# Performance work log

Hardware: AMD Instinct MI355X
Metric: run time of the kernel (lower is better)

The kernel has to match this reference:

```python
import jax, jax.numpy as jnp
import numpy as np

HQ, HKV, D = 16, 2, 128   # num_heads_q, num_heads_kv, head_dim
G = HQ // HKV             # q heads per kv head (repeat_interleave factor)


def setup_inputs() -> dict:
    key = jax.random.key(0)
    ks = jax.random.split(key, 6)
    B, T, C = 2, 2048, 2048
    def w(k, shape):
        return jax.random.normal(k, shape, jnp.float32) * (1.0 / np.sqrt(shape[0]).astype(np.float32))
    x = jax.random.normal(ks[0], (B, T, C), jnp.float32)
    Wq = w(ks[1], (C, HQ * D))
    Wk = w(ks[2], (C, HKV * D))
    Wv = w(ks[3], (C, HKV * D))
    Wo = w(ks[4], (HQ * D, C))
    Wg = w(ks[5], (C, HQ))
    # causal mask: True where attention is disallowed (j > i)
    mask = jnp.triu(jnp.ones((T, T), dtype=bool), k=1)[None, None]  # (1,1,T,T)
    return {"x": x, "mask": mask, "Wq": Wq, "Wk": Wk, "Wv": Wv, "Wo": Wo, "Wg": Wg}


def reference(x, mask, Wq, Wk, Wv, Wo, Wg):
    B, T, C = x.shape
    # repeat_interleave(G, dim=heads) means q head h uses kv head h // G,
    # so group q heads as (HKV, G) instead of materializing repeated K/V.
    q = (x @ Wq).reshape(B, T, HKV, G, D).transpose(0, 2, 3, 1, 4)  # (B,HKV,G,T,D)
    k = (x @ Wk).reshape(B, T, HKV, D).transpose(0, 2, 1, 3)        # (B,HKV,T,D)
    v = (x @ Wv).reshape(B, T, HKV, D).transpose(0, 2, 1, 3)        # (B,HKV,T,D)
    scale = jnp.float32(1.0 / np.sqrt(D))
    scores = jnp.einsum('bkgtd,bksd->bkgts', q, k) * scale          # (B,HKV,G,T,T)
    scores = jnp.where(mask[:, None], jnp.float32(-1e9), scores)    # causal fill
    attn = jax.nn.softmax(scores, axis=-1)
    # post-softmax sigmoid gate, one scalar per (batch, q-head, query token)
    gates = jax.nn.sigmoid(x @ Wg)                                   # (B,T,HQ)
    gates = gates.transpose(0, 2, 1).reshape(B, HKV, G, T)           # (B,HKV,G,T)
    out = jnp.einsum('bkgts,bksd->btkgd', attn * gates[..., None], v)
    out = out.reshape(B, T, HQ * D)
    return out @ Wo
```

## Files before the change

kernel.cpp:

```cpp
#include <hip/hip_runtime.h>
#include <hip/hip_bf16.h>
#include <math.h>

#define HQ 16
#define HKV 2
#define D 128
#define B_SZ 2
#define T_SZ 2048
#define C_SZ 2048
#define QKVN 2688

#define C_Q 0.12753102f
#define C_G 1.44269504f

typedef __attribute__((ext_vector_type(8))) short short8;
typedef __attribute__((ext_vector_type(4))) float floatx4;

static __device__ __forceinline__ float fexp2(float x) {
    return __builtin_amdgcn_exp2f(x);
}

static __device__ __forceinline__ unsigned short f2b(float f) {
    union { float f; unsigned u; } x; x.f = f;
    return (unsigned short)((x.u + 0x7fffu + ((x.u >> 16) & 1u)) >> 16);
}

static __device__ __forceinline__ unsigned int pk2(float a, float b) {
    float2 t; t.x = a; t.y = b;
    __hip_bfloat162 h = __float22bfloat162_rn(t);
    return *(unsigned int*)&h;
}

static __device__ __forceinline__ void load_lds16(const void* g, void* l) {
    __builtin_amdgcn_global_load_lds(
        (const __attribute__((address_space(1))) void*)g,
        (__attribute__((address_space(3))) void*)l,
        16, 0, 0);
}

static __device__ __forceinline__ void tr32(
    const float* __restrict__ in, unsigned short* __restrict__ out,
    int R, int Cc, float premul, int bx, int by, float (*t)[33])
{
    const int bc = bx * 32, br = by * 32;
    const int tid = threadIdx.x;
    const int r = tid >> 3, c4 = (tid & 7) * 4;
    float4 v = *(const float4*)(in + (size_t)(br + r) * Cc + bc + c4);
    t[r][c4 + 0] = v.x; t[r][c4 + 1] = v.y; t[r][c4 + 2] = v.z; t[r][c4 + 3] = v.w;
    __syncthreads();
    ushort4 o;
    o.x = f2b(t[c4 + 0][r] * premul); o.y = f2b(t[c4 + 1][r] * premul);
    o.z = f2b(t[c4 + 2][r] * premul); o.w = f2b(t[c4 + 3][r] * premul);
    *(ushort4*)(out + (size_t)(bc + r) * R + br + c4) = o;
}

__global__ __launch_bounds__(256) void prep_kernel(
    const float* __restrict__ x,  const float* __restrict__ Wq,
    const float* __restrict__ Wk, const float* __restrict__ Wv,
    const float* __restrict__ Wo, const float* __restrict__ Wg,
    unsigned short* __restrict__ xb, unsigned short* __restrict__ Wqkvt,
    unsigned short* __restrict__ Wot)
{
    __shared__ float t[32][33];
    const int bid = blockIdx.x;
    const int tid = threadIdx.x;
    if (bid < 4096) {
        int i = bid * 2048 + tid * 8;
        float4 a = *(const float4*)(x + i);
        float4 b = *(const float4*)(x + i + 4);
        ushort4 o0, o1;
        o0.x = f2b(a.x); o0.y = f2b(a.y); o0.z = f2b(a.z); o0.w = f2b(a.w);
        o1.x = f2b(b.x); o1.y = f2b(b.y); o1.z = f2b(b.z); o1.w = f2b(b.w);
        *(ushort4*)(xb + i) = o0;
        *(ushort4*)(xb + i + 4) = o1;
    } else if (bid < 8192) {
        int n = bid - 4096;
        tr32(Wq, Wqkvt, C_SZ, HQ * D, C_Q, n & 63, n >> 6, t);
    } else if (bid < 8704) {
        int n = bid - 8192;
        tr32(Wk, Wqkvt + (size_t)(HQ * D) * C_SZ, C_SZ, HKV * D, 1.0f, n & 7, n >> 3, t);
    } else if (bid < 9216) {
        int n = bid - 8704;
        tr32(Wv, Wqkvt + (size_t)(HQ * D + HKV * D) * C_SZ, C_SZ, HKV * D, 1.0f, n & 7, n >> 3, t);
    } else if (bid < 13312) {
        int n = bid - 9216;
        tr32(Wo, Wot, HQ * D, C_SZ, 1.0f, n & 63, n >> 6, t);
    } else {
        int k = (bid - 13312) * 256 + tid;
        const float4* wr = (const float4*)(Wg + (size_t)k * 16);
        float4 w0 = wr[0], w1 = wr[1], w2 = wr[2], w3 = wr[3];
        float w[16] = {w0.x, w0.y, w0.z, w0.w, w1.x, w1.y, w1.z, w1.w,
                       w2.x, w2.y, w2.z, w2.w, w3.x, w3.y, w3.z, w3.w};
        unsigned short* out = Wqkvt + (size_t)(HQ * D + 2 * HKV * D) * C_SZ;
        #pragma unroll
        for (int h = 0; h < 16; ++h)
            out[(size_t)h * C_SZ + k] = f2b(w[h] * C_G);
    }
}

template<int BM>
__global__ __launch_bounds__(512, 2) void gemm256(
    const unsigned short* __restrict__ A, const unsigned short* __restrict__ Bt,
    float* __restrict__ Cf, unsigned short* __restrict__ Cb,
    unsigned short* __restrict__ Vt, int Nreal, int K, int out_bf16)
{
    constexpr int MT = BM / 32;
    constexpr int LA = BM / 64;
    constexpr int VM = LA + 4;
    __shared__ __align__(16) unsigned short SM[2][(BM + 256) * 64];

    const int tid = threadIdx.x;
    const int lane = tid & 63, wave = tid >> 6;
    const int l15 = lane & 15, quad = lane >> 4;
    const int wm = wave >> 2, wn = wave & 3;
    const int bm0 = blockIdx.y * BM, bn0 = blockIdx.x * 256;
    const int NT = K >> 6;

    unsigned aoff[LA], boff[4];
    #pragma unroll
    for (int j = 0; j < LA; ++j) {
        int c = j * 512 + tid, r = c >> 3, sb = c & 7;
        aoff[j] = (unsigned)(((bm0 + r) * K + ((sb ^ (r & 7)) << 3)) * 2);
    }
    #pragma unroll
    for (int j = 0; j < 4; ++j) {
        int c = j * 512 + tid, r = c >> 3, sb = c & 7;
        boff[j] = (unsigned)(((bn0 + r) * K + ((sb ^ (r & 7)) << 3)) * 2);
    }

    floatx4 zero = {0.f, 0.f, 0.f, 0.f};
    floatx4 acc[MT][4];
    #pragma unroll
    for (int i = 0; i < MT; ++i)
        #pragma unroll
        for (int j = 0; j < 4; ++j) acc[i][j] = zero;

    auto STAGE = [&](int b, int t) {
        #pragma unroll
        for (int j = 0; j < LA; ++j)
            load_lds16((const char*)A + aoff[j] + (size_t)t * 128,
                       &SM[b][(j * 512 + wave * 64) * 8]);
        #pragma unroll
        for (int j = 0; j < 4; ++j)
            load_lds16((const char*)Bt + boff[j] + (size_t)t * 128,
                       &SM[b][BM * 64 + (j * 512 + wave * 64) * 8]);
    };

    auto RD = [&](short8 (&FA)[MT], short8 (&FB)[4], int b, int kk) {
        const unsigned short* Sa = &SM[b][0];
        const unsigned short* Sb = &SM[b][BM * 64];
        const int swz = ((kk << 2) + quad) ^ (l15 & 7);
        #pragma unroll
        for (int mt = 0; mt < MT; ++mt)
            FA[mt] = *(const short8*)&Sa[(wm * (BM / 2) + mt * 16 + l15) * 64 + swz * 8];
        #pragma unroll
        for (int nt = 0; nt < 4; ++nt)
            FB[nt] = *(const short8*)&Sb[(wn * 64 + nt * 16 + l15) * 64 + swz * 8];
    };

    auto MM = [&](short8 (&FA)[MT], short8 (&FB)[4]) {
        __builtin_amdgcn_s_setprio(1);
        #pragma unroll
        for (int mt = 0; mt < MT; ++mt)
            #pragma unroll
            for (int nt = 0; nt < 4; ++nt)
                acc[mt][nt] = __builtin_amdgcn_mfma_f32_16x16x32_bf16(
                    FA[mt], FB[nt], acc[mt][nt], 0, 0, 0);
        __builtin_amdgcn_s_setprio(0);
    };

    short8 RaA[MT], RaB[4], RbA[MT], RbB[4];

    STAGE(0, 0);
    STAGE(1, 1);
    asm volatile("s_waitcnt vmcnt(%0)" :: "n"(VM) : "memory");
    __builtin_amdgcn_sched_barrier(0);
    __builtin_amdgcn_s_barrier();
    __builtin_amdgcn_sched_barrier(0);
    RD(RaA, RaB, 0, 0);

    #pragma unroll 2
    for (int t = 0; t < NT; ++t) {
        const int b = t & 1;
        RD(RbA, RbB, b, 1);
        MM(RaA, RaB);
        asm volatile("s_waitcnt lgkmcnt(0)" ::: "memory");
        __builtin_amdgcn_sched_barrier(0);
        __builtin_amdgcn_s_barrier();
        __builtin_amdgcn_sched_barrier(0);
        if (t + 2 < NT) {
            STAGE(b, t + 2);
            asm volatile("s_waitcnt vmcnt(%0)" :: "n"(VM) : "memory");
        } else if (t + 1 < NT) {
            asm volatile("s_waitcnt vmcnt(0)" ::: "memory");
        }
        __builtin_amdgcn_sched_barrier(0);
        __builtin_amdgcn_s_barrier();
        __builtin_amdgcn_sched_barrier(0);
        if (t + 1 < NT) RD(RaA, RaB, b ^ 1, 0);
        MM(RbA, RbB);
    }

    if (Vt != nullptr && bn0 == 2304) {
        unsigned short (*Ct)[264] = (unsigned short(*)[264])SM;
        const int bb = bm0 >> 11;
        const int tl = bm0 & 2047;
        #pragma unroll
        for (int v = 0; v < 4; ++v) {
            __syncthreads();
            if (wn == v) {
                #pragma unroll
                for (int mt = 0; mt < MT; ++mt)
                    #pragma unroll
                    for (int nt = 0; nt < 4; ++nt)
                        #pragma unroll
                        for (int r = 0; r < 4; ++r)
                            Ct[nt * 16 + l15][wm * (BM / 2) + mt * 16 + quad * 4 + r] =
                                f2b(acc[mt][nt][r]);
            }
            __syncthreads();
            int row = tid >> 3, c0 = (tid & 7) * 32;
            unsigned short* dst = Vt + ((size_t)bb * (HKV * D) + v * 64 + row) * T_SZ
                                     + tl + c0;
            const unsigned short* src = &Ct[row][c0];
            short8 s0 = *(const short8*)(src + 0);
            short8 s1 = *(const short8*)(src + 8);
            short8 s2 = *(const short8*)(src + 16);
            short8 s3 = *(const short8*)(src + 24);
            *(short8*)(dst + 0)  = s0; *(short8*)(dst + 8)  = s1;
            *(short8*)(dst + 16) = s2; *(short8*)(dst + 24) = s3;
        }
        return;
    }

    #pragma unroll
    for (int mt = 0; mt < MT; ++mt)
        #pragma unroll
        for (int nt = 0; nt < 4; ++nt) {
            const int n = bn0 + wn * 64 + nt * 16 + l15;
            if (n < Nreal) {
                #pragma unroll
                for (int r = 0; r < 4; ++r) {
                    const int m = bm0 + wm * (BM / 2) + mt * 16 + quad * 4 + r;
                    if (out_bf16) Cb[(size_t)m * Nreal + n] = f2b(acc[mt][nt][r]);
                    else          Cf[(size_t)m * Nreal + n] = acc[mt][nt][r];
                }
            }
        }
}

__global__ __launch_bounds__(256, 3) void attn_mfma(
    const unsigned short* __restrict__ QKV, const unsigned short* __restrict__ Vt,
    unsigned short* __restrict__ Ob)
{
    __shared__ __align__(16) unsigned short SMEM[64 * 128 + 128 * 64 + 4 * 16 * 72];
    unsigned short* Ks = SMEM;
    unsigned short* Vs = SMEM + 64 * 128;
    unsigned short* Ps = SMEM + 64 * 128 + 128 * 64;
    unsigned short* Lo = SMEM;

    const int bh = blockIdx.x;
    const int qt = (int)gridDim.y - 1 - (int)blockIdx.y;
    const int b = bh >> 4, h = bh & 15, kvh = h >> 3;
    const int tid = threadIdx.x;
    const int lane = tid & 63, w = tid >> 6;
    const int l15 = lane & 15, quad = lane >> 4;
    const int q_local = w * 16 + l15;
    const float BIAS = 32.0f;

    short8 aq[4];
    {
        const unsigned short* qp = QKV + (size_t)(b * T_SZ + qt * 64 + q_local) * QKVN
                                       + h * D + quad * 8;
        #pragma unroll
        for (int kd = 0; kd < 4; ++kd) aq[kd] = *(const short8*)(qp + kd * 32);
    }

    const unsigned short* kg[4];
    const unsigned short* vg[4];
    #pragma unroll
    for (int it = 0; it < 4; ++it) {
        int Bi = it * 256 + tid;
        int kr = Bi >> 4, kc = ((Bi & 15) ^ (kr & 15)) * 8;
        kg[it] = QKV + (size_t)(b * T_SZ + kr) * QKVN + HQ * D + kvh * D + kc;
        int vr = Bi >> 3, vc = ((Bi & 7) ^ (vr & 7)) * 8;
        vg[it] = Vt + (size_t)((b * HKV + kvh) * D + vr) * T_SZ + vc;
    }

    floatx4 zero = {0.f, 0.f, 0.f, 0.f};
    floatx4 oacc[8];
    #pragma unroll
    for (int dt = 0; dt < 8; ++dt) oacc[dt] = zero;
    float l_part = 0.f;

    short8 krg[4], vrg[4];
    #pragma unroll
    for (int it = 0; it < 4; ++it) {
        krg[it] = *(const short8*)(kg[it]);
        vrg[it] = *(const short8*)(vg[it]);
    }

    for (int kt = 0; kt <= qt; ++kt) {
        asm volatile("s_waitcnt vmcnt(0)" ::: "memory");
        __builtin_amdgcn_sched_barrier(0);
        __builtin_amdgcn_s_barrier();
        __builtin_amdgcn_sched_barrier(0);
        #pragma unroll
        for (int it = 0; it < 4; ++it) {
            *(short8*)&Ks[(it * 256 + tid) * 8] = krg[it];
            *(short8*)&Vs[(it * 256 + tid) * 8] = vrg[it];
        }
        if (kt < qt) {
            #pragma unroll
            for (int it = 0; it < 4; ++it) {
                krg[it] = *(const short8*)(kg[it] + (size_t)(kt + 1) * 64 * QKVN);
                vrg[it] = *(const short8*)(vg[it] + (kt + 1) * 64);
            }
        }
        asm volatile("s_waitcnt lgkmcnt(0)" ::: "memory");
        __builtin_amdgcn_sched_barrier(0);
        __builtin_amdgcn_s_barrier();
        __builtin_amdgcn_sched_barrier(0);

        floatx4 sacc[4];
        #pragma unroll
        for (int nt = 0; nt < 4; ++nt) sacc[nt] = zero;
        #pragma unroll
        for (int kd = 0; kd < 4; ++kd)
            #pragma unroll
            for (int nt = 0; nt < 4; ++nt) {
                short8 ak = *(const short8*)&Ks[((nt * 16 + l15) * 16 + ((kd * 4 + quad) ^ l15)) * 8];
                sacc[nt] = __builtin_amdgcn_mfma_f32_16x16x32_bf16(ak, aq[kd], sacc[nt], 0, 0, 0);
            }

        float p[4][4];
        if (kt == qt) {
            #pragma unroll
            for (int nt = 0; nt < 4; ++nt)
                #pragma unroll
                for (int r = 0; r < 4; ++r) {
                    float e = fexp2(sacc[nt][r] - BIAS);
                    p[nt][r] = (nt * 16 + quad * 4 + r > q_local) ? 0.f : e;
                }
        } else {
            #pragma unroll
            for (int nt = 0; nt < 4; ++nt)
                #pragma unroll
                for (int r = 0; r < 4; ++r)
                    p[nt][r] = fexp2(sacc[nt][r] - BIAS);
        }
        #pragma unroll
        for (int nt = 0; nt < 4; ++nt) {
            l_part += (p[nt][0] + p[nt][1]) + (p[nt][2] + p[nt][3]);
            uint2 pw;
            pw.x = pk2(p[nt][0], p[nt][1]);
            pw.y = pk2(p[nt][2], p[nt][3]);
            *(uint2*)&Ps[(w * 16 + l15) * 72 + nt * 16 + quad * 4] = pw;
        }

        #pragma unroll
        for (int kk = 0; kk < 2; ++kk) {
            short8 bp = *(const short8*)&Ps[(w * 16 + l15) * 72 + kk * 32 + quad * 8];
            #pragma unroll
            for (int dt = 0; dt < 8; ++dt) {
                short8 av = *(const short8*)&Vs[((dt * 16 + l15) * 8 + ((kk * 4 + quad) ^ (l15 & 7))) * 8];
                oacc[dt] = __builtin_amdgcn_mfma_f32_16x16x32_bf16(av, bp, oacc[dt], 0, 0, 0);
            }
        }
    }

    float l = l_part;
    l += __shfl_xor(l, 16);
    l += __shfl_xor(l, 32);

    __syncthreads();
    {
        int token = b * T_SZ + qt * 64 + q_local;
        unsigned short gl = QKV[(size_t)token * QKVN + HQ * D + HKV * D * 2 + h];
        union { unsigned u; float f; } gx; gx.u = ((unsigned)gl) << 16;
        float g = 1.0f / (1.0f + fexp2(-gx.f));
        float f = g / l;
        #pragma unroll
        for (int dt = 0; dt < 8; ++dt) {
            uint2 ov;
            ov.x = pk2(oacc[dt][0] * f, oacc[dt][1] * f);
            ov.y = pk2(oacc[dt][2] * f, oacc[dt][3] * f);
            *(uint2*)&Lo[(size_t)q_local * 136 + dt * 16 + quad * 4] = ov;
        }
    }
    __syncthreads();
    {
        int row = tid >> 2, c0 = (tid & 3) * 32;
        size_t tok = (size_t)(b * T_SZ + qt * 64 + row);
        unsigned short* op = Ob + tok * (HQ * D) + h * D + c0;
        const unsigned short* lp = &Lo[(size_t)row * 136 + c0];
        short8 v0 = *(const short8*)(lp + 0);
        short8 v1 = *(const short8*)(lp + 8);
        short8 v2 = *(const short8*)(lp + 16);
        short8 v3 = *(const short8*)(lp + 24);
        *(short8*)(op + 0)  = v0; *(short8*)(op + 8)  = v1;
        *(short8*)(op + 16) = v2; *(short8*)(op + 24) = v3;
    }
}

extern "C" void kernel_launch(void* const* d_in, const int* in_sizes, int n_in,
                              void* d_out, int out_size, void* d_ws, size_t ws_size,
                              hipStream_t stream) {
    const float* x  = (const float*)d_in[0];
    const float* Wq = (const float*)d_in[2];
    const float* Wk = (const float*)d_in[3];
    const float* Wv = (const float*)d_in[4];
    const float* Wo = (const float*)d_in[5];
    const float* Wg = (const float*)d_in[6];
    float* out = (float*)d_out;

    const size_t KB = 1ull << 10;
    char* p = (char*)d_ws;
    unsigned short* xb    = (unsigned short*)(p);
    unsigned short* Ob    = xb;
    unsigned short* Wqkvt = (unsigned short*)(p + 16384 * KB);
    unsigned short* Wot   = (unsigned short*)(p + 27136 * KB);
    unsigned short* QKV   = (unsigned short*)(p + 35328 * KB);
    unsigned short* Vt    = (unsigned short*)(p + 56832 * KB);
    const int BT = B_SZ * T_SZ;

    prep_kernel<<<dim3(13320), 256, 0, stream>>>(x, Wq, Wk, Wv, Wo, Wg, xb, Wqkvt, Wot);

    gemm256<256><<<dim3(11, BT / 256), 512, 0, stream>>>(
        xb, Wqkvt, nullptr, QKV, Vt, QKVN, C_SZ, 1);

    attn_mfma<<<dim3(B_SZ * HQ, T_SZ / 64), 256, 0, stream>>>(QKV, Vt, Ob);

    gemm256<128><<<dim3(C_SZ / 256, BT / 128), 512, 0, stream>>>(
        Ob, Wot, out, nullptr, nullptr, C_SZ, HQ * D, 0);
}
```

Measured before the change: 289.8 us.

## Restructure GEMM into quadrant ping-pong pipeline and load attention K/V directly to LDS

The GEMM kernel is rebuilt so each K step is split into four quadrant MFMA phases. Loads for the next A and B halves are interleaved between those phases, and workgroup IDs are remapped so neighbouring tiles land on the same XCD. The attention kernel drops its register prefetch of K/V and instead issues direct global-to-LDS loads each iteration, with its occupancy hint relaxed. This aims to overlap global traffic with MFMA work and improve L2 locality in the GEMMs. In exchange it adds many more barriers per step, and the attention loop no longer overlaps the next tile's fetch with compute.

```diff
diff --git a/kernel.cpp b/kernel.cpp
--- a/kernel.cpp
+++ b/kernel.cpp
@@ -37,6 +37,8 @@
         (__attribute__((address_space(3))) void*)l,
         16, 0, 0);
 }
+
+#define SBAR __builtin_amdgcn_sched_barrier(0)
 
 static __device__ __forceinline__ void tr32(
     const float* __restrict__ in, unsigned short* __restrict__ out,
@@ -99,34 +101,54 @@
 }
 
 template<int BM>
-__global__ __launch_bounds__(512, 2) void gemm256(
+__global__ __launch_bounds__(512, 2) void gemm8p(
     const unsigned short* __restrict__ A, const unsigned short* __restrict__ Bt,
     float* __restrict__ Cf, unsigned short* __restrict__ Cb,
     unsigned short* __restrict__ Vt, int Nreal, int K, int out_bf16)
 {
     constexpr int MT = BM / 32;
-    constexpr int LA = BM / 64;
+    constexpr int MH = MT / 2;
+    constexpr int LA = BM / 128;
+    constexpr int AUNIT = (BM / 2) * 64;
+    constexpr int BUNIT = 8192;
+    constexpr int BUF = 2 * AUNIT + 2 * BUNIT;
     constexpr int VM = LA + 4;
-    __shared__ __align__(16) unsigned short SM[2][(BM + 256) * 64];
+    __shared__ __align__(16) unsigned short SM[2][BUF];
 
     const int tid = threadIdx.x;
     const int lane = tid & 63, wave = tid >> 6;
     const int l15 = lane & 15, quad = lane >> 4;
     const int wm = wave >> 2, wn = wave & 3;
-    const int bm0 = blockIdx.y * BM, bn0 = blockIdx.x * 256;
     const int NT = K >> 6;
 
-    unsigned aoff[LA], boff[4];
-    #pragma unroll
-    for (int j = 0; j < LA; ++j) {
-        int c = j * 512 + tid, r = c >> 3, sb = c & 7;
-        aoff[j] = (unsigned)(((bm0 + r) * K + ((sb ^ (r & 7)) << 3)) * 2);
-    }
-    #pragma unroll
-    for (int j = 0; j < 4; ++j) {
-        int c = j * 512 + tid, r = c >> 3, sb = c & 7;
-        boff[j] = (unsigned)(((bn0 + r) * K + ((sb ^ (r & 7)) << 3)) * 2);
-    }
+    const int nwg = (int)(gridDim.x * gridDim.y);
+    int flat = (int)(blockIdx.y * gridDim.x + blockIdx.x);
+    const int cpx = nwg >> 3;
+    flat = (flat & 7) * cpx + (flat >> 3);
+    const int bm0 = (flat / (int)gridDim.x) * BM;
+    const int bn0 = (flat % (int)gridDim.x) * 256;
+
+    const int rr = tid >> 3;
+    const int cb8 = ((tid & 7) ^ (rr & 7)) << 3;
+    unsigned aoff[2][LA], boff[2][2];
+    #pragma unroll
+    for (int mh = 0; mh < 2; ++mh)
+        #pragma unroll
+        for (int j = 0; j < LA; ++j) {
+            int row_l = j * 64 + rr;
+            int grow;
+            if (BM == 256) grow = bm0 + (row_l >> 6) * 128 + mh * 64 + (row_l & 63);
+            else           grow = bm0 + (row_l >> 5) * 64  + mh * 32 + (row_l & 31);
+            aoff[mh][j] = (unsigned)((grow * K + cb8) * 2);
+        }
+    #pragma unroll
+    for (int nh = 0; nh < 2; ++nh)
+        #pragma unroll
+        for (int j = 0; j < 2; ++j) {
+            int row_l = j * 64 + rr;
+            int gnr = bn0 + (row_l >> 5) * 64 + nh * 32 + (row_l & 31);
+            boff[nh][j] = (unsigned)((gnr * K + cb8) * 2);
+        }
 
     floatx4 zero = {0.f, 0.f, 0.f, 0.f};
     floatx4 acc[MT][4];
@@ -135,73 +157,93 @@
         #pragma unroll
         for (int j = 0; j < 4; ++j) acc[i][j] = zero;
 
-    auto STAGE = [&](int b, int t) {
+    auto STAGE_A = [&](int b, int mh, int t) {
         #pragma unroll
         for (int j = 0; j < LA; ++j)
-            load_lds16((const char*)A + aoff[j] + (size_t)t * 128,
-                       &SM[b][(j * 512 + wave * 64) * 8]);
-        #pragma unroll
-        for (int j = 0; j < 4; ++j)
-            load_lds16((const char*)Bt + boff[j] + (size_t)t * 128,
-                       &SM[b][BM * 64 + (j * 512 + wave * 64) * 8]);
+            load_lds16((const char*)A + aoff[mh][j] + (size_t)t * 128,
+                       &SM[b][mh * AUNIT + (j * 512 + wave * 64) * 8]);
     };
-
-    auto RD = [&](short8 (&FA)[MT], short8 (&FB)[4], int b, int kk) {
-        const unsigned short* Sa = &SM[b][0];
-        const unsigned short* Sb = &SM[b][BM * 64];
-        const int swz = ((kk << 2) + quad) ^ (l15 & 7);
-        #pragma unroll
-        for (int mt = 0; mt < MT; ++mt)
-            FA[mt] = *(const short8*)&Sa[(wm * (BM / 2) + mt * 16 + l15) * 64 + swz * 8];
-        #pragma unroll
-        for (int nt = 0; nt < 4; ++nt)
-            FB[nt] = *(const short8*)&Sb[(wn * 64 + nt * 16 + l15) * 64 + swz * 8];
+    auto STAGE_B = [&](int b, int nh, int t) {
+        #pragma unroll
+        for (int j = 0; j < 2; ++j)
+            load_lds16((const char*)Bt + boff[nh][j] + (size_t)t * 128,
+                       &SM[b][2 * AUNIT + nh * BUNIT + (j * 512 + wave * 64) * 8]);
     };
 
-    auto MM = [&](short8 (&FA)[MT], short8 (&FB)[4]) {
+    short8 fa[MH][2], fb[4][2];
+    auto RD_A = [&](int b, int mh) {
+        const unsigned short* Sa = &SM[b][mh * AUNIT];
+        #pragma unroll
+        for (int i = 0; i < MH; ++i) {
+            const int row_l = wm * (BM / 4) + i * 16 + l15;
+            #pragma unroll
+            for (int kk = 0; kk < 2; ++kk)
+                fa[i][kk] = *(const short8*)&Sa[row_l * 64 +
+                    ((((kk << 2) + quad) ^ (l15 & 7)) << 3)];
+        }
+    };
+    auto RD_Bh = [&](int b, int nh) {
+        const unsigned short* Sb = &SM[b][2 * AUNIT + nh * BUNIT];
+        #pragma unroll
+        for (int s = 0; s < 2; ++s) {
+            const int row_l = wn * 32 + s * 16 + l15;
+            #pragma unroll
+            for (int kk = 0; kk < 2; ++kk)
+                fb[nh * 2 + s][kk] = *(const short8*)&Sb[row_l * 64 +
+                    ((((kk << 2) + quad) ^ (l15 & 7)) << 3)];
+        }
+    };
+    auto MMQ = [&](int mh, int nh) {
         __builtin_amdgcn_s_setprio(1);
         #pragma unroll
-        for (int mt = 0; mt < MT; ++mt)
-            #pragma unroll
-            for (int nt = 0; nt < 4; ++nt)
-                acc[mt][nt] = __builtin_amdgcn_mfma_f32_16x16x32_bf16(
-                    FA[mt], FB[nt], acc[mt][nt], 0, 0, 0);
+        for (int i = 0; i < MH; ++i)
+            #pragma unroll
+            for (int s = 0; s < 2; ++s)
+                #pragma unroll
+                for (int kk = 0; kk < 2; ++kk)
+                    acc[mh * MH + i][nh * 2 + s] = __builtin_amdgcn_mfma_f32_16x16x32_bf16(
+                        fa[i][kk], fb[nh * 2 + s][kk], acc[mh * MH + i][nh * 2 + s], 0, 0, 0);
         __builtin_amdgcn_s_setprio(0);
     };
 
-    short8 RaA[MT], RaB[4], RbA[MT], RbB[4];
-
-    STAGE(0, 0);
-    STAGE(1, 1);
+    STAGE_A(0, 0, 0); STAGE_B(0, 0, 0); STAGE_B(0, 1, 0); STAGE_A(0, 1, 0);
+    if (NT > 1) { STAGE_A(1, 0, 1); STAGE_B(1, 0, 1); STAGE_B(1, 1, 1); }
     asm volatile("s_waitcnt vmcnt(%0)" :: "n"(VM) : "memory");
-    __builtin_amdgcn_sched_barrier(0);
-    __builtin_amdgcn_s_barrier();
-    __builtin_amdgcn_sched_barrier(0);
-    RD(RaA, RaB, 0, 0);
+    SBAR; __builtin_amdgcn_s_barrier(); SBAR;
 
     #pragma unroll 2
     for (int t = 0; t < NT; ++t) {
         const int b = t & 1;
-        RD(RbA, RbB, b, 1);
-        MM(RaA, RaB);
-        asm volatile("s_waitcnt lgkmcnt(0)" ::: "memory");
-        __builtin_amdgcn_sched_barrier(0);
-        __builtin_amdgcn_s_barrier();
-        __builtin_amdgcn_sched_barrier(0);
+        RD_A(b, 0); RD_Bh(b, 0);
+        if (t + 1 < NT) STAGE_A(b ^ 1, 1, t + 1);
+        SBAR; __builtin_amdgcn_s_barrier(); SBAR;
+        asm volatile("s_waitcnt lgkmcnt(0)" ::: "memory"); SBAR;
+        MMQ(0, 0);
+        SBAR; __builtin_amdgcn_s_barrier(); SBAR;
+        RD_Bh(b, 1);
+        if (t + 2 < NT) STAGE_A(b, 0, t + 2);
+        SBAR; __builtin_amdgcn_s_barrier(); SBAR;
+        asm volatile("s_waitcnt lgkmcnt(0)" ::: "memory"); SBAR;
+        MMQ(0, 1);
+        SBAR; __builtin_amdgcn_s_barrier(); SBAR;
+        RD_A(b, 1);
+        if (t + 2 < NT) STAGE_B(b, 0, t + 2);
+        SBAR; __builtin_amdgcn_s_barrier(); SBAR;
+        asm volatile("s_waitcnt lgkmcnt(0)" ::: "memory"); SBAR;
+        MMQ(1, 1);
+        SBAR; __builtin_amdgcn_s_barrier(); SBAR;
         if (t + 2 < NT) {
-            STAGE(b, t + 2);
+            STAGE_B(b, 1, t + 2);
             asm volatile("s_waitcnt vmcnt(%0)" :: "n"(VM) : "memory");
-        } else if (t + 1 < NT) {
+        } else {
             asm volatile("s_waitcnt vmcnt(0)" ::: "memory");
         }
-        __builtin_amdgcn_sched_barrier(0);
-        __builtin_amdgcn_s_barrier();
-        __builtin_amdgcn_sched_barrier(0);
-        if (t + 1 < NT) RD(RaA, RaB, b ^ 1, 0);
-        MM(RbA, RbB);
-    }
-
-    if (Vt != nullptr && bn0 == 2304) {
+        SBAR; __builtin_amdgcn_s_barrier(); SBAR;
+        MMQ(1, 0);
+        SBAR; __builtin_amdgcn_s_barrier(); SBAR;
+    }
+
+    if (BM == 256 && Vt != nullptr && bn0 == 2304) {
         unsigned short (*Ct)[264] = (unsigned short(*)[264])SM;
         const int bb = bm0 >> 11;
         const int tl = bm0 & 2047;
@@ -249,7 +291,7 @@
         }
 }
 
-__global__ __launch_bounds__(256, 3) void attn_mfma(
+__global__ __launch_bounds__(256) void attn_mfma(
     const unsigned short* __restrict__ QKV, const unsigned short* __restrict__ Vt,
     unsigned short* __restrict__ Ob)
 {
@@ -293,34 +335,14 @@
     for (int dt = 0; dt < 8; ++dt) oacc[dt] = zero;
     float l_part = 0.f;
 
-    short8 krg[4], vrg[4];
-    #pragma unroll
-    for (int it = 0; it < 4; ++it) {
-        krg[it] = *(const short8*)(kg[it]);
-        vrg[it] = *(const short8*)(vg[it]);
-    }
-
     for (int kt = 0; kt <= qt; ++kt) {
-        asm volatile("s_waitcnt vmcnt(0)" ::: "memory");
-        __builtin_amdgcn_sched_barrier(0);
-        __builtin_amdgcn_s_barrier();
-        __builtin_amdgcn_sched_barrier(0);
+        __syncthreads();
         #pragma unroll
         for (int it = 0; it < 4; ++it) {
-            *(short8*)&Ks[(it * 256 + tid) * 8] = krg[it];
-            *(short8*)&Vs[(it * 256 + tid) * 8] = vrg[it];
-        }
-        if (kt < qt) {
-            #pragma unroll
-            for (int it = 0; it < 4; ++it) {
-                krg[it] = *(const short8*)(kg[it] + (size_t)(kt + 1) * 64 * QKVN);
-                vrg[it] = *(const short8*)(vg[it] + (kt + 1) * 64);
-            }
-        }
-        asm volatile("s_waitcnt lgkmcnt(0)" ::: "memory");
-        __builtin_amdgcn_sched_barrier(0);
-        __builtin_amdgcn_s_barrier();
-        __builtin_amdgcn_sched_barrier(0);
+            load_lds16(kg[it] + (size_t)kt * 64 * QKVN, &Ks[(it * 256 + w * 64) * 8]);
+            load_lds16(vg[it] + kt * 64,                &Vs[(it * 256 + w * 64) * 8]);
+        }
+        __syncthreads();
 
         floatx4 sacc[4];
         #pragma unroll
@@ -426,11 +448,11 @@
 
     prep_kernel<<<dim3(13320), 256, 0, stream>>>(x, Wq, Wk, Wv, Wo, Wg, xb, Wqkvt, Wot);
 
-    gemm256<256><<<dim3(11, BT / 256), 512, 0, stream>>>(
+    gemm8p<256><<<dim3(11, BT / 256), 512, 0, stream>>>(
         xb, Wqkvt, nullptr, QKV, Vt, QKVN, C_SZ, 1);
 
     attn_mfma<<<dim3(B_SZ * HQ, T_SZ / 64), 256, 0, stream>>>(QKV, Vt, Ob);
 
-    gemm256<128><<<dim3(C_SZ / 256, BT / 128), 512, 0, stream>>>(
+    gemm8p<128><<<dim3(8, BT / 128), 512, 0, stream>>>(
         Ob, Wot, out, nullptr, nullptr, C_SZ, HQ * D, 0);
 }
```

Result: faster. 282.8 us (-2.4%).
